# Kernel tuning notes

Measured on AMD Instinct MI355X. Metric: run time of the kernel, lower is better.

The kernel has to match this reference:

```python
import jax, jax.numpy as jnp
import numpy as np

B, I, D = 16384, 128, 16  # batch, input_size, n_dim


def setup_inputs() -> dict:
    key = jax.random.key(0)
    ks = jax.random.split(key, 14)
    inp = {
        "h": jax.random.normal(ks[0], (B, I * D), dtype=jnp.float32),
        "X": jax.random.normal(ks[1], (B, I), dtype=jnp.float32),
        "M": jax.random.uniform(ks[2], (B, I), dtype=jnp.float32),
        "gamma_h": jax.random.uniform(ks[3], (B, I, D), dtype=jnp.float32),
        "W_r": jax.random.normal(ks[4], (I, 1, D), dtype=jnp.float32),
        "W_z": jax.random.normal(ks[5], (I, 1, D), dtype=jnp.float32),
        "W_h": jax.random.normal(ks[6], (I, 1, D), dtype=jnp.float32),
        "U_r": jax.random.normal(ks[7], (I, D, D), dtype=jnp.float32),
        "U_z": jax.random.normal(ks[8], (I, D, D), dtype=jnp.float32),
        "U_h": jax.random.normal(ks[9], (I, D, D), dtype=jnp.float32),
        "V_r": jax.random.normal(ks[10], (I, 1, D), dtype=jnp.float32),
        "V_z": jax.random.normal(ks[11], (I, 1, D), dtype=jnp.float32),
        "V_h": jax.random.normal(ks[12], (I, 1, D), dtype=jnp.float32),
        "b_r": jnp.zeros((I, D), dtype=jnp.float32),
        "b_z": jnp.zeros((I, D), dtype=jnp.float32),
        "b_h": jnp.zeros((I, D), dtype=jnp.float32),
    }
    return inp


def reference(h, X, M, gamma_h, W_r, W_z, W_h, U_r, U_z, U_h,
              V_r, V_z, V_h, b_r, b_z, b_h):
    b = X.shape[0]
    i, d = W_r.shape[0], W_r.shape[2]
    # decayed hidden state, per-feature blocks: [B, I, D]
    hh = h.reshape(b, i, d) * gamma_h
    # X/M contributions: X is [B, I]; W/V are [I, 1, D] -> outer product per feature
    xr = jnp.einsum('bi,id->bid', X, W_r[:, 0, :])
    xz = jnp.einsum('bi,id->bid', X, W_z[:, 0, :])
    xh = jnp.einsum('bi,id->bid', X, W_h[:, 0, :])
    mr = jnp.einsum('bi,id->bid', M, V_r[:, 0, :])
    mz = jnp.einsum('bi,id->bid', M, V_z[:, 0, :])
    mh = jnp.einsum('bi,id->bid', M, V_h[:, 0, :])
    # per-feature small matmuls on hidden blocks
    r = jax.nn.sigmoid(xr + jnp.einsum('bid,ide->bie', hh, U_r) + mr + b_r)
    z = jax.nn.sigmoid(xz + jnp.einsum('bid,ide->bie', hh, U_z) + mz + b_z)
    h_tilde = jnp.tanh(xh + jnp.einsum('bid,ide->bie', r * hh, U_h) + mh + b_h)
    out = z * hh + (1.0 - z) * h_tilde
    return out.reshape(b, i * d)
```

## Files before the change

kernel.cpp:

```cpp
#include <hip/hip_runtime.h>
#include <hip/hip_bf16.h>


typedef float  f32x4_t  __attribute__((ext_vector_type(4)));
typedef short  bf16x8_t __attribute__((ext_vector_type(8)));

constexpr int I_TOT = 128;
constexpr int ROWL  = 2048;
constexpr int SW    = 516;

__device__ __forceinline__ unsigned short bf16_rne(float x) {
    union { float f; unsigned u; } c; c.f = x;
    unsigned u = c.u + 0x7fffu + ((c.u >> 16) & 1u);
    return (unsigned short)(u >> 16);
}
__device__ __forceinline__ float bf16_to_f(unsigned short b) {
    union { float f; unsigned u; } c; c.u = ((unsigned)b) << 16;
    return c.f;
}
__device__ __forceinline__ float fast_sigmoid(float x) {
    float e = __expf(-x);
    return __builtin_amdgcn_rcpf(1.0f + e);
}
__device__ __forceinline__ float fast_tanh(float x) {
    x = fminf(fmaxf(x, -10.0f), 10.0f);
    float e = __expf(-2.0f * x);
    return (1.0f - e) * __builtin_amdgcn_rcpf(1.0f + e);
}

struct BPair { bf16x8_t hi, lo; };

__device__ __forceinline__ BPair build_b(float u0, float u1, float u2, float u3) {
    unsigned short h0 = bf16_rne(u0), h1 = bf16_rne(u1),
                   h2 = bf16_rne(u2), h3 = bf16_rne(u3);
    unsigned short l0 = bf16_rne(u0 - bf16_to_f(h0));
    unsigned short l1 = bf16_rne(u1 - bf16_to_f(h1));
    unsigned short l2 = bf16_rne(u2 - bf16_to_f(h2));
    unsigned short l3 = bf16_rne(u3 - bf16_to_f(h3));
    BPair p;
    p.hi[0] = (short)h0; p.hi[1] = (short)h1; p.hi[2] = (short)h2; p.hi[3] = (short)h3;
    p.hi[4] = (short)h0; p.hi[5] = (short)h1; p.hi[6] = (short)h2; p.hi[7] = (short)h3;
    p.lo[0] = (short)l0; p.lo[1] = (short)l1; p.lo[2] = (short)l2; p.lo[3] = (short)l3;
    p.lo[4] = 0; p.lo[5] = 0; p.lo[6] = 0; p.lo[7] = 0;
    return p;
}

__device__ __forceinline__ bf16x8_t build_a(float a0, float a1, float a2, float a3) {
    unsigned short h0 = bf16_rne(a0), h1 = bf16_rne(a1),
                   h2 = bf16_rne(a2), h3 = bf16_rne(a3);
    unsigned short l0 = bf16_rne(a0 - bf16_to_f(h0));
    unsigned short l1 = bf16_rne(a1 - bf16_to_f(h1));
    unsigned short l2 = bf16_rne(a2 - bf16_to_f(h2));
    unsigned short l3 = bf16_rne(a3 - bf16_to_f(h3));
    bf16x8_t A;
    A[0] = (short)h0; A[1] = (short)h1; A[2] = (short)h2; A[3] = (short)h3;
    A[4] = (short)l0; A[5] = (short)l1; A[6] = (short)l2; A[7] = (short)l3;
    return A;
}

__device__ __forceinline__ f32x4_t mm(bf16x8_t a, bf16x8_t b, f32x4_t c) {
    return __builtin_amdgcn_mfma_f32_16x16x32_bf16(a, b, c, 0, 0, 0);
}

__global__ __launch_bounds__(256)
__attribute__((amdgpu_waves_per_eu(3, 8)))
void gru_d_mfma(
    const float* __restrict__ h,
    const float* __restrict__ X,
    const float* __restrict__ M,
    const float* __restrict__ gam,
    const float* __restrict__ W_r, const float* __restrict__ W_z, const float* __restrict__ W_h,
    const float* __restrict__ U_r, const float* __restrict__ U_z, const float* __restrict__ U_h,
    const float* __restrict__ V_r, const float* __restrict__ V_z, const float* __restrict__ V_h,
    const float* __restrict__ b_r, const float* __restrict__ b_z, const float* __restrict__ b_h,
    float* __restrict__ out)
{
    __shared__ __align__(16) float shh[16 * SW];

    const int t  = threadIdx.x;
    const int w  = t >> 6;
    const int l  = t & 63;
    const int bi = l & 15;
    const int dA = (l >> 4) * 4;

    const int b0 = blockIdx.y * 16;
    const int i0 = blockIdx.x * 32;

    {
        const int r0 = 4 * w;
#define STAGE(rr)                                                             \
        {                                                                     \
            const size_t gb = (size_t)(b0 + r0 + (rr)) * ROWL + i0 * 16;      \
            float4 h0 = *reinterpret_cast<const float4*>(h   + gb + 4 * l);   \
            float4 h1 = *reinterpret_cast<const float4*>(h   + gb + 256 + 4 * l); \
            float4 g0 = *reinterpret_cast<const float4*>(gam + gb + 4 * l);   \
            float4 g1 = *reinterpret_cast<const float4*>(gam + gb + 256 + 4 * l); \
            float4 p0, p1;                                                    \
            p0.x = h0.x * g0.x; p0.y = h0.y * g0.y;                           \
            p0.z = h0.z * g0.z; p0.w = h0.w * g0.w;                           \
            p1.x = h1.x * g1.x; p1.y = h1.y * g1.y;                           \
            p1.z = h1.z * g1.z; p1.w = h1.w * g1.w;                           \
            *reinterpret_cast<float4*>(&shh[(r0 + (rr)) * SW + 4 * l]) = p0;  \
            *reinterpret_cast<float4*>(&shh[(r0 + (rr)) * SW + 256 + 4 * l]) = p1; \
        }
        STAGE(0) STAGE(1) STAGE(2) STAGE(3)
#undef STAGE
    }
    __syncthreads();

    const int iw0 = i0 + w * 8;
    const size_t orow = (size_t)(b0 + bi) * ROWL + dA;
    const size_t xrow = (size_t)(b0 + bi) * I_TOT;

    float4 phh = *reinterpret_cast<const float4*>(&shh[bi * SW + (w * 8) * 16 + dA]);
    float px = X[xrow + iw0];
    float pm = M[xrow + iw0];
    const float* Urp = U_r + iw0 * 256 + bi;
    const float* Uzp = U_z + iw0 * 256 + bi;
    const float* Uhp = U_h + iw0 * 256 + bi;
    float pur0 = Urp[(dA+0)*16], pur1 = Urp[(dA+1)*16],
          pur2 = Urp[(dA+2)*16], pur3 = Urp[(dA+3)*16];
    float puz0 = Uzp[(dA+0)*16], puz1 = Uzp[(dA+1)*16],
          puz2 = Uzp[(dA+2)*16], puz3 = Uzp[(dA+3)*16];
    float puh0 = Uhp[(dA+0)*16], puh1 = Uhp[(dA+1)*16],
          puh2 = Uhp[(dA+2)*16], puh3 = Uhp[(dA+3)*16];

    #pragma unroll
    for (int it = 0; it < 8; ++it) {
        const int i    = iw0 + it;
        const int itpf = (it + 1) & 7;
        const int ipf  = iw0 + itpf;

        float4 nhh = *reinterpret_cast<const float4*>(
            &shh[bi * SW + (w * 8 + itpf) * 16 + dA]);
        float nx = X[xrow + ipf];
        float nm = M[xrow + ipf];
        const float* nUr = U_r + ipf * 256 + bi;
        const float* nUz = U_z + ipf * 256 + bi;
        const float* nUh = U_h + ipf * 256 + bi;
        float nur0 = nUr[(dA+0)*16], nur1 = nUr[(dA+1)*16],
              nur2 = nUr[(dA+2)*16], nur3 = nUr[(dA+3)*16];
        float nuz0 = nUz[(dA+0)*16], nuz1 = nUz[(dA+1)*16],
              nuz2 = nUz[(dA+2)*16], nuz3 = nUz[(dA+3)*16];
        float nuh0 = nUh[(dA+0)*16], nuh1 = nUh[(dA+1)*16],
              nuh2 = nUh[(dA+2)*16], nuh3 = nUh[(dA+3)*16];

        const float4 wr4 = *reinterpret_cast<const float4*>(W_r + i*16 + dA);
        const float4 wz4 = *reinterpret_cast<const float4*>(W_z + i*16 + dA);
        const float4 wh4 = *reinterpret_cast<const float4*>(W_h + i*16 + dA);
        const float4 vr4 = *reinterpret_cast<const float4*>(V_r + i*16 + dA);
        const float4 vz4 = *reinterpret_cast<const float4*>(V_z + i*16 + dA);
        const float4 vh4 = *reinterpret_cast<const float4*>(V_h + i*16 + dA);
        const float4 br4 = *reinterpret_cast<const float4*>(b_r + i*16 + dA);
        const float4 bz4 = *reinterpret_cast<const float4*>(b_z + i*16 + dA);
        const float4 bh4 = *reinterpret_cast<const float4*>(b_h + i*16 + dA);

        BPair Br = build_b(pur0, pur1, pur2, pur3);
        BPair Bz = build_b(puz0, puz1, puz2, puz3);
        BPair Bh = build_b(puh0, puh1, puh2, puh3);

        float hh0 = phh.x, hh1 = phh.y, hh2 = phh.z, hh3 = phh.w;
        bf16x8_t Ahh = build_a(hh0, hh1, hh2, hh3);

        f32x4_t accR, accZ, accH;
        accR[0] = 0.f; accR[1] = 0.f; accR[2] = 0.f; accR[3] = 0.f;
        accZ[0] = 0.f; accZ[1] = 0.f; accZ[2] = 0.f; accZ[3] = 0.f;
        accR = mm(Br.hi, Ahh, accR); accR = mm(Br.lo, Ahh, accR);
        accZ = mm(Bz.hi, Ahh, accZ); accZ = mm(Bz.lo, Ahh, accZ);

        float rh0 = fast_sigmoid(accR[0] + fmaf(px, wr4.x, fmaf(pm, vr4.x, br4.x))) * hh0;
        float rh1 = fast_sigmoid(accR[1] + fmaf(px, wr4.y, fmaf(pm, vr4.y, br4.y))) * hh1;
        float rh2 = fast_sigmoid(accR[2] + fmaf(px, wr4.z, fmaf(pm, vr4.z, br4.z))) * hh2;
        float rh3 = fast_sigmoid(accR[3] + fmaf(px, wr4.w, fmaf(pm, vr4.w, br4.w))) * hh3;
        bf16x8_t Arh = build_a(rh0, rh1, rh2, rh3);

        accH[0] = 0.f; accH[1] = 0.f; accH[2] = 0.f; accH[3] = 0.f;
        accH = mm(Bh.hi, Arh, accH); accH = mm(Bh.lo, Arh, accH);

        float4 o;
        {
            float z0 = fast_sigmoid(accZ[0] + fmaf(px, wz4.x, fmaf(pm, vz4.x, bz4.x)));
            float t0 = fast_tanh(accH[0] + fmaf(px, wh4.x, fmaf(pm, vh4.x, bh4.x)));
            o.x = fmaf(z0, hh0 - t0, t0);
            float z1 = fast_sigmoid(accZ[1] + fmaf(px, wz4.y, fmaf(pm, vz4.y, bz4.y)));
            float t1 = fast_tanh(accH[1] + fmaf(px, wh4.y, fmaf(pm, vh4.y, bh4.y)));
            o.y = fmaf(z1, hh1 - t1, t1);
            float z2 = fast_sigmoid(accZ[2] + fmaf(px, wz4.z, fmaf(pm, vz4.z, bz4.z)));
            float t2 = fast_tanh(accH[2] + fmaf(px, wh4.z, fmaf(pm, vh4.z, bh4.z)));
            o.z = fmaf(z2, hh2 - t2, t2);
            float z3 = fast_sigmoid(accZ[3] + fmaf(px, wz4.w, fmaf(pm, vz4.w, bz4.w)));
            float t3 = fast_tanh(accH[3] + fmaf(px, wh4.w, fmaf(pm, vh4.w, bh4.w)));
            o.w = fmaf(z3, hh3 - t3, t3);
        }
        *reinterpret_cast<float4*>(out + orow + (size_t)i * 16) = o;

        phh = nhh; px = nx; pm = nm;
        pur0 = nur0; pur1 = nur1; pur2 = nur2; pur3 = nur3;
        puz0 = nuz0; puz1 = nuz1; puz2 = nuz2; puz3 = nuz3;
        puh0 = nuh0; puh1 = nuh1; puh2 = nuh2; puh3 = nuh3;
    }
}

extern "C" void kernel_launch(void* const* d_in, const int* in_sizes, int n_in,
                              void* d_out, int out_size, void* d_ws, size_t ws_size,
                              hipStream_t stream) {
    const float* h       = (const float*)d_in[0];
    const float* X       = (const float*)d_in[1];
    const float* M       = (const float*)d_in[2];
    const float* gamma_h = (const float*)d_in[3];
    const float* W_r     = (const float*)d_in[4];
    const float* W_z     = (const float*)d_in[5];
    const float* W_h     = (const float*)d_in[6];
    const float* U_r     = (const float*)d_in[7];
    const float* U_z     = (const float*)d_in[8];
    const float* U_h     = (const float*)d_in[9];
    const float* V_r     = (const float*)d_in[10];
    const float* V_z     = (const float*)d_in[11];
    const float* V_h     = (const float*)d_in[12];
    const float* b_r     = (const float*)d_in[13];
    const float* b_z     = (const float*)d_in[14];
    const float* b_h     = (const float*)d_in[15];
    float* out = (float*)d_out;

    dim3 grid(I_TOT / 32, 16384 / 16);
    dim3 block(256);
    gru_d_mfma<<<grid, block, 0, stream>>>(h, X, M, gamma_h,
                                           W_r, W_z, W_h,
                                           U_r, U_z, U_h,
                                           V_r, V_z, V_h,
                                           b_r, b_z, b_h,
                                           out);
}
```

Baseline: 119.3 us.

## Drop U low-part MFMAs, fold input terms into accumulator init, trim prefetch

Removes the bf16 low-residual split for the U weight matrices, so each gate needs one MFMA instead of two. The X/M/bias contributions now seed the MFMA accumulator directly instead of being added after it. The wasted wrap-around prefetch on the last iteration is skipped, and bf16 conversion uses the HIP intrinsic. This cuts MFMA count and conversion ALU work, at the cost of lower precision in U (bf16 only), which raises the error relative to the fp32 reference.

```diff
diff --git a/kernel.cpp b/kernel.cpp
--- a/kernel.cpp
+++ b/kernel.cpp
@@ -9,10 +9,10 @@
 constexpr int ROWL  = 2048;
 constexpr int SW    = 516;
 
-__device__ __forceinline__ unsigned short bf16_rne(float x) {
-    union { float f; unsigned u; } c; c.f = x;
-    unsigned u = c.u + 0x7fffu + ((c.u >> 16) & 1u);
-    return (unsigned short)(u >> 16);
+__device__ __forceinline__ unsigned short bf16c(float x) {
+    union { __hip_bfloat16 b; unsigned short u; } cv;
+    cv.b = __float2bfloat16(x);
+    return cv.u;
 }
 __device__ __forceinline__ float bf16_to_f(unsigned short b) {
     union { float f; unsigned u; } c; c.u = ((unsigned)b) << 16;
@@ -28,34 +28,26 @@
     return (1.0f - e) * __builtin_amdgcn_rcpf(1.0f + e);
 }
 
-struct BPair { bf16x8_t hi, lo; };
-
-__device__ __forceinline__ BPair build_b(float u0, float u1, float u2, float u3) {
-    unsigned short h0 = bf16_rne(u0), h1 = bf16_rne(u1),
-                   h2 = bf16_rne(u2), h3 = bf16_rne(u3);
-    unsigned short l0 = bf16_rne(u0 - bf16_to_f(h0));
-    unsigned short l1 = bf16_rne(u1 - bf16_to_f(h1));
-    unsigned short l2 = bf16_rne(u2 - bf16_to_f(h2));
-    unsigned short l3 = bf16_rne(u3 - bf16_to_f(h3));
-    BPair p;
-    p.hi[0] = (short)h0; p.hi[1] = (short)h1; p.hi[2] = (short)h2; p.hi[3] = (short)h3;
-    p.hi[4] = (short)h0; p.hi[5] = (short)h1; p.hi[6] = (short)h2; p.hi[7] = (short)h3;
-    p.lo[0] = (short)l0; p.lo[1] = (short)l1; p.lo[2] = (short)l2; p.lo[3] = (short)l3;
-    p.lo[4] = 0; p.lo[5] = 0; p.lo[6] = 0; p.lo[7] = 0;
-    return p;
-}
-
 __device__ __forceinline__ bf16x8_t build_a(float a0, float a1, float a2, float a3) {
-    unsigned short h0 = bf16_rne(a0), h1 = bf16_rne(a1),
-                   h2 = bf16_rne(a2), h3 = bf16_rne(a3);
-    unsigned short l0 = bf16_rne(a0 - bf16_to_f(h0));
-    unsigned short l1 = bf16_rne(a1 - bf16_to_f(h1));
-    unsigned short l2 = bf16_rne(a2 - bf16_to_f(h2));
-    unsigned short l3 = bf16_rne(a3 - bf16_to_f(h3));
+    unsigned short h0 = bf16c(a0), h1 = bf16c(a1),
+                   h2 = bf16c(a2), h3 = bf16c(a3);
+    unsigned short l0 = bf16c(a0 - bf16_to_f(h0));
+    unsigned short l1 = bf16c(a1 - bf16_to_f(h1));
+    unsigned short l2 = bf16c(a2 - bf16_to_f(h2));
+    unsigned short l3 = bf16c(a3 - bf16_to_f(h3));
     bf16x8_t A;
     A[0] = (short)h0; A[1] = (short)h1; A[2] = (short)h2; A[3] = (short)h3;
     A[4] = (short)l0; A[5] = (short)l1; A[6] = (short)l2; A[7] = (short)l3;
     return A;
+}
+
+__device__ __forceinline__ bf16x8_t build_u(float u0, float u1, float u2, float u3) {
+    unsigned short h0 = bf16c(u0), h1 = bf16c(u1),
+                   h2 = bf16c(u2), h3 = bf16c(u3);
+    bf16x8_t B;
+    B[0] = (short)h0; B[1] = (short)h1; B[2] = (short)h2; B[3] = (short)h3;
+    B[4] = (short)h0; B[5] = (short)h1; B[6] = (short)h2; B[7] = (short)h3;
+    return B;
 }
 
 __device__ __forceinline__ f32x4_t mm(bf16x8_t a, bf16x8_t b, f32x4_t c) {
@@ -127,23 +119,7 @@
 
     #pragma unroll
     for (int it = 0; it < 8; ++it) {
-        const int i    = iw0 + it;
-        const int itpf = (it + 1) & 7;
-        const int ipf  = iw0 + itpf;
-
-        float4 nhh = *reinterpret_cast<const float4*>(
-            &shh[bi * SW + (w * 8 + itpf) * 16 + dA]);
-        float nx = X[xrow + ipf];
-        float nm = M[xrow + ipf];
-        const float* nUr = U_r + ipf * 256 + bi;
-        const float* nUz = U_z + ipf * 256 + bi;
-        const float* nUh = U_h + ipf * 256 + bi;
-        float nur0 = nUr[(dA+0)*16], nur1 = nUr[(dA+1)*16],
-              nur2 = nUr[(dA+2)*16], nur3 = nUr[(dA+3)*16];
-        float nuz0 = nUz[(dA+0)*16], nuz1 = nUz[(dA+1)*16],
-              nuz2 = nUz[(dA+2)*16], nuz3 = nUz[(dA+3)*16];
-        float nuh0 = nUh[(dA+0)*16], nuh1 = nUh[(dA+1)*16],
-              nuh2 = nUh[(dA+2)*16], nuh3 = nUh[(dA+3)*16];
+        const int i = iw0 + it;
 
         const float4 wr4 = *reinterpret_cast<const float4*>(W_r + i*16 + dA);
         const float4 wz4 = *reinterpret_cast<const float4*>(W_z + i*16 + dA);
@@ -155,49 +131,75 @@
         const float4 bz4 = *reinterpret_cast<const float4*>(b_z + i*16 + dA);
         const float4 bh4 = *reinterpret_cast<const float4*>(b_h + i*16 + dA);
 
-        BPair Br = build_b(pur0, pur1, pur2, pur3);
-        BPair Bz = build_b(puz0, puz1, puz2, puz3);
-        BPair Bh = build_b(puh0, puh1, puh2, puh3);
+        bf16x8_t BUr = build_u(pur0, pur1, pur2, pur3);
+        bf16x8_t BUz = build_u(puz0, puz1, puz2, puz3);
+        bf16x8_t BUh = build_u(puh0, puh1, puh2, puh3);
 
         float hh0 = phh.x, hh1 = phh.y, hh2 = phh.z, hh3 = phh.w;
         bf16x8_t Ahh = build_a(hh0, hh1, hh2, hh3);
 
-        f32x4_t accR, accZ, accH;
-        accR[0] = 0.f; accR[1] = 0.f; accR[2] = 0.f; accR[3] = 0.f;
-        accZ[0] = 0.f; accZ[1] = 0.f; accZ[2] = 0.f; accZ[3] = 0.f;
-        accR = mm(Br.hi, Ahh, accR); accR = mm(Br.lo, Ahh, accR);
-        accZ = mm(Bz.hi, Ahh, accZ); accZ = mm(Bz.lo, Ahh, accZ);
-
-        float rh0 = fast_sigmoid(accR[0] + fmaf(px, wr4.x, fmaf(pm, vr4.x, br4.x))) * hh0;
-        float rh1 = fast_sigmoid(accR[1] + fmaf(px, wr4.y, fmaf(pm, vr4.y, br4.y))) * hh1;
-        float rh2 = fast_sigmoid(accR[2] + fmaf(px, wr4.z, fmaf(pm, vr4.z, br4.z))) * hh2;
-        float rh3 = fast_sigmoid(accR[3] + fmaf(px, wr4.w, fmaf(pm, vr4.w, br4.w))) * hh3;
+        float4 nhh; float nx, nm;
+        float nur0, nur1, nur2, nur3, nuz0, nuz1, nuz2, nuz3, nuh0, nuh1, nuh2, nuh3;
+        if (it < 7) {
+            const int ipf = i + 1;
+            nhh = *reinterpret_cast<const float4*>(
+                &shh[bi * SW + (w * 8 + it + 1) * 16 + dA]);
+            nx = X[xrow + ipf];
+            nm = M[xrow + ipf];
+            const float* nUr = U_r + ipf * 256 + bi;
+            const float* nUz = U_z + ipf * 256 + bi;
+            const float* nUh = U_h + ipf * 256 + bi;
+            nur0 = nUr[(dA+0)*16]; nur1 = nUr[(dA+1)*16];
+            nur2 = nUr[(dA+2)*16]; nur3 = nUr[(dA+3)*16];
+            nuz0 = nUz[(dA+0)*16]; nuz1 = nUz[(dA+1)*16];
+            nuz2 = nUz[(dA+2)*16]; nuz3 = nUz[(dA+3)*16];
+            nuh0 = nUh[(dA+0)*16]; nuh1 = nUh[(dA+1)*16];
+            nuh2 = nUh[(dA+2)*16]; nuh3 = nUh[(dA+3)*16];
+        }
+
+        f32x4_t initR, initZ, initH;
+        initR[0] = fmaf(px, wr4.x, fmaf(pm, vr4.x, br4.x));
+        initR[1] = fmaf(px, wr4.y, fmaf(pm, vr4.y, br4.y));
+        initR[2] = fmaf(px, wr4.z, fmaf(pm, vr4.z, br4.z));
+        initR[3] = fmaf(px, wr4.w, fmaf(pm, vr4.w, br4.w));
+        initZ[0] = fmaf(px, wz4.x, fmaf(pm, vz4.x, bz4.x));
+        initZ[1] = fmaf(px, wz4.y, fmaf(pm, vz4.y, bz4.y));
+        initZ[2] = fmaf(px, wz4.z, fmaf(pm, vz4.z, bz4.z));
+        initZ[3] = fmaf(px, wz4.w, fmaf(pm, vz4.w, bz4.w));
+        f32x4_t accR = mm(BUr, Ahh, initR);
+        f32x4_t accZ = mm(BUz, Ahh, initZ);
+
+        float rh0 = fast_sigmoid(accR[0]) * hh0;
+        float rh1 = fast_sigmoid(accR[1]) * hh1;
+        float rh2 = fast_sigmoid(accR[2]) * hh2;
+        float rh3 = fast_sigmoid(accR[3]) * hh3;
         bf16x8_t Arh = build_a(rh0, rh1, rh2, rh3);
 
-        accH[0] = 0.f; accH[1] = 0.f; accH[2] = 0.f; accH[3] = 0.f;
-        accH = mm(Bh.hi, Arh, accH); accH = mm(Bh.lo, Arh, accH);
+        initH[0] = fmaf(px, wh4.x, fmaf(pm, vh4.x, bh4.x));
+        initH[1] = fmaf(px, wh4.y, fmaf(pm, vh4.y, bh4.y));
+        initH[2] = fmaf(px, wh4.z, fmaf(pm, vh4.z, bh4.z));
+        initH[3] = fmaf(px, wh4.w, fmaf(pm, vh4.w, bh4.w));
+        f32x4_t accH = mm(BUh, Arh, initH);
 
         float4 o;
         {
-            float z0 = fast_sigmoid(accZ[0] + fmaf(px, wz4.x, fmaf(pm, vz4.x, bz4.x)));
-            float t0 = fast_tanh(accH[0] + fmaf(px, wh4.x, fmaf(pm, vh4.x, bh4.x)));
+            float z0 = fast_sigmoid(accZ[0]); float t0 = fast_tanh(accH[0]);
             o.x = fmaf(z0, hh0 - t0, t0);
-            float z1 = fast_sigmoid(accZ[1] + fmaf(px, wz4.y, fmaf(pm, vz4.y, bz4.y)));
-            float t1 = fast_tanh(accH[1] + fmaf(px, wh4.y, fmaf(pm, vh4.y, bh4.y)));
+            float z1 = fast_sigmoid(accZ[1]); float t1 = fast_tanh(accH[1]);
             o.y = fmaf(z1, hh1 - t1, t1);
-            float z2 = fast_sigmoid(accZ[2] + fmaf(px, wz4.z, fmaf(pm, vz4.z, bz4.z)));
-            float t2 = fast_tanh(accH[2] + fmaf(px, wh4.z, fmaf(pm, vh4.z, bh4.z)));
+            float z2 = fast_sigmoid(accZ[2]); float t2 = fast_tanh(accH[2]);
             o.z = fmaf(z2, hh2 - t2, t2);
-            float z3 = fast_sigmoid(accZ[3] + fmaf(px, wz4.w, fmaf(pm, vz4.w, bz4.w)));
-            float t3 = fast_tanh(accH[3] + fmaf(px, wh4.w, fmaf(pm, vh4.w, bh4.w)));
+            float z3 = fast_sigmoid(accZ[3]); float t3 = fast_tanh(accH[3]);
             o.w = fmaf(z3, hh3 - t3, t3);
         }
         *reinterpret_cast<float4*>(out + orow + (size_t)i * 16) = o;
 
-        phh = nhh; px = nx; pm = nm;
-        pur0 = nur0; pur1 = nur1; pur2 = nur2; pur3 = nur3;
-        puz0 = nuz0; puz1 = nuz1; puz2 = nuz2; puz3 = nuz3;
-        puh0 = nuh0; puh1 = nuh1; puh2 = nuh2; puh3 = nuh3;
+        if (it < 7) {
+            phh = nhh; px = nx; pm = nm;
+            pur0 = nur0; pur1 = nur1; pur2 = nur2; pur3 = nur3;
+            puz0 = nuz0; puz1 = nuz1; puz2 = nuz2; puz3 = nuz3;
+            puh0 = nuh0; puh1 = nuh1; puh2 = nuh2; puh3 = nuh3;
+        }
     }
 }
 
```

Measured after the change: 114.2 us. -4.2%, faster.
